# Performance work log

Measured on AMD Instinct MI355X. Metric: run time of the kernel, lower is better.

Reference implementation:

```python
import jax, jax.numpy as jnp
import numpy as np

H = 768   # encoder hidden size
NH = 4    # boundary attention heads
HD = H // NH
E = 9     # ent_type_size
R = 12    # rel_type_size
D = 64    # inner_dim
B = 4
S = 1024


def setup_inputs() -> dict:
    key = jax.random.key(0)
    ks = jax.random.split(key, 8)
    n = lambda k, shp: jax.random.normal(k, shp, jnp.float32) * 0.02
    return dict(
        hidden_states=jax.random.normal(ks[0], (B, S, H), jnp.float32),
        attention_mask=jnp.ones((B, S), jnp.float32),
        in_proj_w=n(ks[1], (3 * H, H)), in_proj_b=jnp.zeros((3 * H,), jnp.float32),
        out_proj_w=n(ks[2], (H, H)), out_proj_b=jnp.zeros((H,), jnp.float32),
        gate_w=n(ks[3], (H, H)), gate_b=jnp.zeros((H,), jnp.float32),
        ln_g=jnp.ones((H,), jnp.float32), ln_b=jnp.zeros((H,), jnp.float32),
        ent_w=n(ks[4], (E * 2 * D, H)), ent_b=jnp.zeros((E * 2 * D,), jnp.float32),
        prior_w=n(ks[5], (H, E)), prior_b=jnp.zeros((H,), jnp.float32),
        rel_w=n(ks[6], (R * 2 * D, 2 * H)), rel_b=jnp.zeros((R * 2 * D,), jnp.float32),
    )


def _sinusoidal_pos_emb(seq_len, dim, dtype):
    pos = jnp.arange(seq_len, dtype=dtype)[:, None]                 # [S,1]
    inv = jnp.power(jnp.asarray(10000.0, dtype), -2.0 * jnp.arange(dim // 2, dtype=dtype) / dim)
    ang = pos * inv                                                  # [S,D/2]
    emb = jnp.stack([jnp.sin(ang), jnp.cos(ang)], axis=-1).reshape(seq_len, dim)  # [sin0,cos0,sin1,cos1,...]
    return emb


def _gp_matrix(hs, W, b, mask):
    # hs: [B,S,Hin], W: [T*2D, Hin], mask: [B,S]
    bsz, seq_len, _ = hs.shape
    out = hs @ W.T + b                                               # [B,S,T*2D]
    T = out.shape[-1] // (2 * D)
    out = out.reshape(bsz, seq_len, T, 2 * D)
    qw, kw = out[..., :D], out[..., D:]                              # [B,S,T,D]
    # RoPE
    pe = _sinusoidal_pos_emb(seq_len, D, hs.dtype)                   # [S,D]
    cos = jnp.repeat(pe[:, 1::2], 2, axis=-1)[None, :, None, :]      # [1,S,1,D]
    sin = jnp.repeat(pe[:, ::2], 2, axis=-1)[None, :, None, :]

    def rot(x):
        x2 = jnp.stack([-x[..., 1::2], x[..., ::2]], axis=-1).reshape(x.shape)
        return x * cos + x2 * sin

    qw, kw = rot(qw), rot(kw)
    logits = jnp.einsum('bmtd,bntd->btmn', qw, kw)                   # [B,T,S,S]
    pad = mask[:, None, None, :]                                     # masks key dim
    logits = logits * pad - (1.0 - pad) * 1e12
    tril = jnp.tril(jnp.ones((seq_len, seq_len), logits.dtype), -1)
    logits = logits - tril * 1e12                                    # strictly lower triangle masked
    return logits / jnp.sqrt(jnp.asarray(D, logits.dtype))


def _boundary_attention(hs, mask, in_proj_w, in_proj_b, out_proj_w, out_proj_b,
                        gate_w, gate_b, ln_g, ln_b):
    bsz, seq_len, _ = hs.shape
    qkv = hs @ in_proj_w.T + in_proj_b                               # [B,S,3H]
    q, k, v = jnp.split(qkv, 3, axis=-1)
    q = q.reshape(bsz, seq_len, NH, HD)
    k = k.reshape(bsz, seq_len, NH, HD)
    v = v.reshape(bsz, seq_len, NH, HD)
    scores = jnp.einsum('bqhd,bkhd->bhqk', q, k) / jnp.sqrt(jnp.asarray(HD, hs.dtype))
    key_pad = (mask == 0)[:, None, None, :]                          # [B,1,1,S]
    scores = jnp.where(key_pad, jnp.asarray(-1e9, hs.dtype), scores)
    attn = jax.nn.softmax(scores, axis=-1)
    ctx = jnp.einsum('bhqk,bkhd->bqhd', attn, v).reshape(bsz, seq_len, H)
    attn_out = ctx @ out_proj_w.T + out_proj_b
    gate = jax.nn.sigmoid(attn_out @ gate_w.T + gate_b)
    x = hs + gate * attn_out
    mu = jnp.mean(x, axis=-1, keepdims=True)
    var = jnp.var(x, axis=-1, keepdims=True)
    return (x - mu) / jnp.sqrt(var + 1e-5) * ln_g + ln_b


def reference(hidden_states, attention_mask, in_proj_w, in_proj_b, out_proj_w, out_proj_b,
              gate_w, gate_b, ln_g, ln_b, ent_w, ent_b, prior_w, prior_b, rel_w, rel_b):
    enhanced = _boundary_attention(hidden_states, attention_mask, in_proj_w, in_proj_b,
                                   out_proj_w, out_proj_b, gate_w, gate_b, ln_g, ln_b)
    ent_logits = _gp_matrix(enhanced, ent_w, ent_b, attention_mask)  # [B,E,S,S]
    ent_prior = jnp.max(ent_logits, axis=-1)                          # [B,E,S]
    ent_prior = jnp.swapaxes(ent_prior, 1, 2)                         # [B,S,E]
    prior_feat = jax.nn.relu(ent_prior @ prior_w.T + prior_b)         # [B,S,H]
    rel_hidden = jnp.concatenate([enhanced, prior_feat], axis=-1)     # [B,S,2H]
    rel_logits = _gp_matrix(rel_hidden, rel_w, rel_b, attention_mask) # [B,R,S,S]
    return (ent_logits, rel_logits, enhanced)
```

## Files before the change

### kernel.cpp

```cpp
#include <hip/hip_runtime.h>
#include <math.h>

#define H_   768
#define NH_  4
#define HD_  192
#define E_   9
#define R_   12
#define D_   64
#define B_   4
#define S_   1024
#define H3_  (3 * H_)
#define MBS_ (B_ * S_)

typedef unsigned short u16;
typedef __attribute__((ext_vector_type(4))) int   i32x4;
typedef __attribute__((ext_vector_type(4))) float f32x4;

static const long OUT_REL_OFF = (long)B_ * E_ * S_ * S_;
static const long OUT_ENH_OFF = OUT_REL_OFF + (long)B_ * R_ * S_ * S_;

__device__ __forceinline__ u16 f2bf(float f) {
    unsigned u = __builtin_bit_cast(unsigned, f);
    return (u16)((u + 0x7fffu + ((u >> 16) & 1u)) >> 16);
}
__device__ __forceinline__ float bf2f(u16 h) {
    return __builtin_bit_cast(float, (unsigned)h << 16);
}
__device__ __forceinline__ void gload16(const u16* g, u16* l) {
    __builtin_amdgcn_global_load_lds(
        (__attribute__((address_space(1))) void*)g,
        (__attribute__((address_space(3))) void*)l, 16, 0, 0);
}
__device__ __forceinline__ void mfma_bf16(f32x4& acc, i32x4 a, i32x4 b) {
    asm volatile("v_mfma_f32_16x16x32_bf16 %0, %1, %2, %0"
                 : "+v"(acc) : "v"(a), "v"(b));
}

template<int BM, int BN, int EPI, int OBF, int PIPE>
__global__ __launch_bounds__(256) void gemm_mfma(
    const u16* __restrict__ A, const u16* __restrict__ Bw,
    const float* __restrict__ bias, void* __restrict__ Cv,
    int K, int lda, int ldb, int ldc, int nh,
    long sAb, long sAh, long sBb, long sBh, long sCb, long sCh,
    const float* __restrict__ mask, float scale, float* __restrict__ aux)
{
    constexpr int MI = BM / 32, NJ = BN / 32;
    constexpr int BUFE = (BM + BN) * 64;
    constexpr int LPS  = BM / 32 + BN / 32;
    const int z = blockIdx.z;
    const int zb = z / nh, zh = z - zb * nh;
    A  += zb * sAb + zh * sAh;
    Bw += zb * sBb + zh * sBh;

    const int gx = gridDim.x, gy = gridDim.y;
    int id = blockIdx.y * gx + blockIdx.x;
    const int nwg = gx * gy;
    if ((nwg & 7) == 0) id = (id & 7) * (nwg >> 3) + (id >> 3);
    const int bx = id % gx, by = id / gx;
    const int m0 = by * BM, n0 = bx * BN;

    __shared__ u16 lds[(PIPE ? 2 : 1) * BUFE];

    const int t = threadIdx.x;
    const int lane = t & 63, wid = t >> 6;
    const int wr = wid >> 1, wc = wid & 1;
    const int l16 = lane & 15, l4 = lane >> 4;

    auto stage = [&](int kt, u16* la) {
        u16* lb = la + BM * 64;
        const int k0 = kt << 6;
        #pragma unroll
        for (int i = 0; i < BM / 32; ++i) {
            const int e = i * 256 + t;
            const int row = e >> 3;
            const int c = ((e & 7) ^ (row & 7)) << 3;
            gload16(A + (long)(m0 + row) * lda + k0 + c, la + e * 8);
        }
        #pragma unroll
        for (int i = 0; i < BN / 32; ++i) {
            const int e = i * 256 + t;
            const int row = e >> 3;
            const int c = ((e & 7) ^ (row & 7)) << 3;
            gload16(Bw + (long)(n0 + row) * ldb + k0 + c, lb + e * 8);
        }
    };

    f32x4 acc[MI][NJ];
    #pragma unroll
    for (int mi = 0; mi < MI; ++mi)
        #pragma unroll
        for (int nj = 0; nj < NJ; ++nj)
            #pragma unroll
            for (int q = 0; q < 4; ++q) acc[mi][nj][q] = 0.0f;

    const int nt = K >> 6;

    if (PIPE == 0) {
        stage(0, lds);
        __syncthreads();
        const u16* la = lds;
        const u16* lb = lds + BM * 64;
        i32x4 af[MI][2], bfr[NJ][2];
        #pragma unroll
        for (int mi = 0; mi < MI; ++mi)
            #pragma unroll
            for (int kk = 0; kk < 2; ++kk) {
                const int row = wr * (BM / 2) + mi * 16 + l16;
                af[mi][kk] = *(const i32x4*)&la[row * 64 + ((((kk << 2) + l4) ^ (row & 7)) << 3)];
            }
        #pragma unroll
        for (int nj = 0; nj < NJ; ++nj)
            #pragma unroll
            for (int kk = 0; kk < 2; ++kk) {
                const int row = wc * (BN / 2) + nj * 16 + l16;
                bfr[nj][kk] = *(const i32x4*)&lb[row * 64 + ((((kk << 2) + l4) ^ (row & 7)) << 3)];
            }
        #pragma unroll
        for (int kk = 0; kk < 2; ++kk)
            #pragma unroll
            for (int mi = 0; mi < MI; ++mi)
                #pragma unroll
                for (int nj = 0; nj < NJ; ++nj)
                    mfma_bf16(acc[mi][nj], af[mi][kk], bfr[nj][kk]);
    } else {
        stage(0, lds);
        if (nt > 1) stage(1, lds + BUFE);
        for (int tt = 0; tt < nt; ++tt) {
            if (tt + 1 < nt) {
                if constexpr (LPS == 8) asm volatile("s_waitcnt vmcnt(8)" ::: "memory");
                else if constexpr (LPS == 7) asm volatile("s_waitcnt vmcnt(7)" ::: "memory");
                else if constexpr (LPS == 6) asm volatile("s_waitcnt vmcnt(6)" ::: "memory");
                else asm volatile("s_waitcnt vmcnt(5)" ::: "memory");
            } else {
                asm volatile("s_waitcnt vmcnt(0)" ::: "memory");
            }
            __builtin_amdgcn_s_barrier();
            u16* la = lds + (tt & 1) * BUFE;
            const u16* lb = la + BM * 64;
            i32x4 af[MI][2], bfr[NJ][2];
            #pragma unroll
            for (int mi = 0; mi < MI; ++mi)
                #pragma unroll
                for (int kk = 0; kk < 2; ++kk) {
                    const int row = wr * (BM / 2) + mi * 16 + l16;
                    af[mi][kk] = *(const i32x4*)&la[row * 64 + ((((kk << 2) + l4) ^ (row & 7)) << 3)];
                }
            #pragma unroll
            for (int nj = 0; nj < NJ; ++nj)
                #pragma unroll
                for (int kk = 0; kk < 2; ++kk) {
                    const int row = wc * (BN / 2) + nj * 16 + l16;
                    bfr[nj][kk] = *(const i32x4*)&lb[row * 64 + ((((kk << 2) + l4) ^ (row & 7)) << 3)];
                }
            asm volatile("s_waitcnt lgkmcnt(0)" ::: "memory");
            __builtin_amdgcn_sched_barrier(0);
            __builtin_amdgcn_s_barrier();
            if (tt + 2 < nt) stage(tt + 2, la);
            #pragma unroll
            for (int kk = 0; kk < 2; ++kk)
                #pragma unroll
                for (int mi = 0; mi < MI; ++mi)
                    #pragma unroll
                    for (int nj = 0; nj < NJ; ++nj)
                        mfma_bf16(acc[mi][nj], af[mi][kk], bfr[nj][kk]);
        }
        __syncthreads();
    }
    __builtin_amdgcn_sched_barrier(0);
    asm volatile("s_nop 7");
    asm volatile("s_nop 7");
    __builtin_amdgcn_sched_barrier(0);

    if (EPI == 1 || EPI == 3) mask += (long)zb * S_;
    const long cbase = zb * sCb + zh * sCh;

    float red[MI][4];
    if (EPI == 3) {
        #pragma unroll
        for (int mi = 0; mi < MI; ++mi)
            #pragma unroll
            for (int r = 0; r < 4; ++r) red[mi][r] = -INFINITY;
    }

    #pragma unroll
    for (int mi = 0; mi < MI; ++mi) {
        #pragma unroll
        for (int nj = 0; nj < NJ; ++nj) {
            const int gn = n0 + wc * (BN / 2) + nj * 16 + l16;
            const float bv = ((EPI == 0 || EPI == 4 || EPI == 7) && bias) ? bias[gn] : 0.0f;
            float invf = 0.0f;
            if (EPI == 4) invf = exp2f(-(float)((gn & 63) >> 1) * 0.41524101186092503f);
            #pragma unroll
            for (int r = 0; r < 4; ++r) {
                const int gm = m0 + wr * (BM / 2) + mi * 16 + l4 * 4 + r;
                float v = acc[mi][nj][r];
                const long cidx = cbase + (long)gm * ldc + gn;
                if (EPI == 0) {
                    v += bv;
                    if (OBF) ((u16*)Cv)[cidx] = f2bf(v);
                    else     ((float*)Cv)[cidx] = v;
                } else if (EPI == 7) {
                    v += bv;
                    const u16 bfv = f2bf(v);
                    ((u16*)Cv)[cidx] = bfv;
                    if (gn >= 2 * H_) {
                        const int hh = (gn - 2 * H_) / HD_;
                        const int dd = (gn - 2 * H_) - hh * HD_;
                        const int bb = gm >> 10, ss = gm & (S_ - 1);
                        ((u16*)aux)[((long)(bb * NH_ + hh) * HD_ + dd) * S_ + ss] = bfv;
                    }
                } else if (EPI == 1 || EPI == 3) {
                    const float pad = mask[gn];
                    v = v * pad - (1.0f - pad) * 1e12f;
                    if (gm > gn) v -= 1e12f;
                    v *= 0.125f;
                    ((float*)Cv)[cidx] = v;
                    if (EPI == 3) red[mi][r] = fmaxf(red[mi][r], v);
                } else {
                    v += bv;
                    const int sp = gm & (S_ - 1);
                    float sn, cs;
                    __sincosf((float)sp * invf, &sn, &cs);
                    const float pv = __shfl_xor(v, 1, 64);
                    v = (gn & 1) ? fmaf(v, cs, pv * sn) : fmaf(v, cs, -pv * sn);
                    ((u16*)Cv)[cidx] = f2bf(v);
                }
            }
        }
    }

    if (EPI == 3) {
        #pragma unroll
        for (int mi = 0; mi < MI; ++mi) {
            #pragma unroll
            for (int r = 0; r < 4; ++r) {
                float m = red[mi][r];
                m = fmaxf(m, __shfl_xor(m, 1, 64));
                m = fmaxf(m, __shfl_xor(m, 2, 64));
                m = fmaxf(m, __shfl_xor(m, 4, 64));
                m = fmaxf(m, __shfl_xor(m, 8, 64));
                if (l16 == 0) {
                    const int gm = m0 + wr * (BM / 2) + mi * 16 + l4 * 4 + r;
                    aux[((long)z * S_ + gm) * 16 + bx * 2 + wc] = m;
                }
            }
        }
    }
}

__global__ __launch_bounds__(256) void attn_fused(
    const u16* __restrict__ qkv, const u16* __restrict__ vt,
    const float* __restrict__ mask, u16* __restrict__ ctx, float qscale)
{
    const int z = blockIdx.y;
    const int b = z >> 2, h = z & 3;
    const int s0 = blockIdx.x * 64;
    const int t = threadIdx.x;
    const int lane = t & 63, wid = t >> 6;
    const int wr = wid >> 1, wc = wid & 1;
    const int l16 = lane & 15, l4 = lane >> 4;

    __shared__ u16 k_lds[64 * 192];
    __shared__ u16 v_lds[192 * 64];
    __shared__ u16 p_lds[64 * 64];
    __shared__ float rs_lds[2][64];

    i32x4 qf[2][6];
    {
        const u16* qb = qkv + (long)(b * S_ + s0 + wr * 32 + l16) * H3_ + h * HD_;
        #pragma unroll
        for (int mi = 0; mi < 2; ++mi)
            #pragma unroll
            for (int kk = 0; kk < 6; ++kk)
                qf[mi][kk] = *(const i32x4*)(qb + (long)mi * 16 * H3_ + kk * 32 + l4 * 8);
    }
    asm volatile("s_waitcnt vmcnt(0)" ::: "memory");

    f32x4 acc_c[2][6];
    #pragma unroll
    for (int mi = 0; mi < 2; ++mi)
        #pragma unroll
        for (int nj = 0; nj < 6; ++nj)
            #pragma unroll
            for (int q = 0; q < 4; ++q) acc_c[mi][nj][q] = 0.0f;
    float rs_acc[2][4] = {};

    const float* mrow = mask + (long)b * S_;

    for (int kt = 0; kt < 16; ++kt) {
        const int kv0 = kt * 64;
        #pragma unroll
        for (int i = 0; i < 6; ++i) {
            const int e = i * 256 + t;
            const int row = e / 24;
            const int g = e - row * 24;
            const int gs = (g & ~7) | ((g & 7) ^ (row & 7));
            gload16(qkv + (long)(b * S_ + kv0 + row) * H3_ + H_ + h * HD_ + gs * 8,
                    k_lds + e * 8);
        }
        #pragma unroll
        for (int i = 0; i < 6; ++i) {
            const int e = i * 256 + t;
            const int row = e >> 3, g = e & 7;
            const int gs = g ^ (row & 7);
            gload16(vt + ((long)z * HD_ + row) * S_ + kv0 + gs * 8,
                    v_lds + e * 8);
        }
        asm volatile("s_waitcnt vmcnt(6)" ::: "memory");
        __builtin_amdgcn_s_barrier();

        f32x4 acc_s[2][2];
        #pragma unroll
        for (int mi = 0; mi < 2; ++mi)
            #pragma unroll
            for (int nj = 0; nj < 2; ++nj)
                #pragma unroll
                for (int q = 0; q < 4; ++q) acc_s[mi][nj][q] = 0.0f;
        #pragma unroll
        for (int kk = 0; kk < 6; ++kk) {
            #pragma unroll
            for (int nj = 0; nj < 2; ++nj) {
                const int row = wc * 32 + nj * 16 + l16;
                const int g = kk * 4 + l4;
                const int gs = (g & ~7) | ((g & 7) ^ (row & 7));
                const i32x4 kf = *(const i32x4*)&k_lds[row * 192 + gs * 8];
                #pragma unroll
                for (int mi = 0; mi < 2; ++mi)
                    mfma_bf16(acc_s[mi][nj], qf[mi][kk], kf);
            }
        }
        __builtin_amdgcn_sched_barrier(0);
        asm volatile("s_nop 7");
        asm volatile("s_nop 7");
        __builtin_amdgcn_sched_barrier(0);

        float rsp[2][4] = {};
        #pragma unroll
        for (int mi = 0; mi < 2; ++mi) {
            #pragma unroll
            for (int nj = 0; nj < 2; ++nj) {
                const int coll = wc * 32 + nj * 16 + l16;
                const float mk = mrow[kv0 + coll];
                #pragma unroll
                for (int r = 0; r < 4; ++r) {
                    const int rowl = wr * 32 + mi * 16 + l4 * 4 + r;
                    float tv = 0.0f;
                    if (mk != 0.0f) tv = __expf(acc_s[mi][nj][r] * qscale);
                    const int gs = (coll >> 3) ^ (rowl & 7);
                    p_lds[rowl * 64 + gs * 8 + (coll & 7)] = f2bf(tv);
                    rsp[mi][r] += tv;
                }
            }
        }
        #pragma unroll
        for (int mi = 0; mi < 2; ++mi)
            #pragma unroll
            for (int r = 0; r < 4; ++r) {
                float v = rsp[mi][r];
                v += __shfl_xor(v, 1, 64);
                v += __shfl_xor(v, 2, 64);
                v += __shfl_xor(v, 4, 64);
                v += __shfl_xor(v, 8, 64);
                rs_acc[mi][r] += v;
            }

        asm volatile("s_waitcnt vmcnt(0)" ::: "memory");
        __builtin_amdgcn_s_barrier();

        #pragma unroll
        for (int kk = 0; kk < 2; ++kk) {
            i32x4 pf[2];
            #pragma unroll
            for (int mi = 0; mi < 2; ++mi) {
                const int row = wr * 32 + mi * 16 + l16;
                const int gs = (kk * 4 + l4) ^ (row & 7);
                pf[mi] = *(const i32x4*)&p_lds[row * 64 + gs * 8];
            }
            #pragma unroll
            for (int nj = 0; nj < 6; ++nj) {
                const int row = wc * 96 + nj * 16 + l16;
                const int gs = (kk * 4 + l4) ^ (row & 7);
                const i32x4 vf = *(const i32x4*)&v_lds[row * 64 + gs * 8];
                #pragma unroll
                for (int mi = 0; mi < 2; ++mi)
                    mfma_bf16(acc_c[mi][nj], pf[mi], vf);
            }
        }
        __builtin_amdgcn_s_barrier();
    }

    __builtin_amdgcn_sched_barrier(0);
    asm volatile("s_nop 7");
    asm volatile("s_nop 7");
    __builtin_amdgcn_sched_barrier(0);

    if (l16 == 0) {
        #pragma unroll
        for (int mi = 0; mi < 2; ++mi)
            #pragma unroll
            for (int r = 0; r < 4; ++r)
                rs_lds[wc][wr * 32 + mi * 16 + l4 * 4 + r] = rs_acc[mi][r];
    }
    __syncthreads();

    #pragma unroll
    for (int mi = 0; mi < 2; ++mi) {
        #pragma unroll
        for (int r = 0; r < 4; ++r) {
            const int rowl = wr * 32 + mi * 16 + l4 * 4 + r;
            const float inv = 1.0f / (rs_lds[0][rowl] + rs_lds[1][rowl]);
            #pragma unroll
            for (int nj = 0; nj < 6; ++nj) {
                const int d = wc * 96 + nj * 16 + l16;
                ctx[(long)(b * S_ + s0 + rowl) * H_ + h * HD_ + d] =
                    f2bf(acc_c[mi][nj][r] * inv);
            }
        }
    }
}

__global__ __launch_bounds__(256) void cast_all(
    const float* __restrict__ hs, const float* __restrict__ ipw,
    const float* __restrict__ opw, const float* __restrict__ gw,
    const float* __restrict__ entw, const float* __restrict__ relw,
    u16* hs_o, u16* ipw_o, u16* opw_o, u16* gw_o, u16* entw_o, u16* relw_o)
{
    const int blk = blockIdx.x;
    const float* in; u16* out; long base;
    if      (blk < 3072) { in = hs;   out = hs_o;   base = (long)blk * 1024; }
    else if (blk < 4800) { in = ipw;  out = ipw_o;  base = (long)(blk - 3072) * 1024; }
    else if (blk < 5376) { in = opw;  out = opw_o;  base = (long)(blk - 4800) * 1024; }
    else if (blk < 5952) { in = gw;   out = gw_o;   base = (long)(blk - 5376) * 1024; }
    else if (blk < 6816) { in = entw; out = entw_o; base = (long)(blk - 5952) * 1024; }
    else                 { in = relw; out = relw_o; base = (long)(blk - 6816) * 1024; }
    const long idx = base + (long)threadIdx.x * 4;
    const float4 v = *(const float4*)&in[idx];
    ushort4 o; o.x = f2bf(v.x); o.y = f2bf(v.y); o.z = f2bf(v.z); o.w = f2bf(v.w);
    *(ushort4*)&out[idx] = o;
}

__global__ __launch_bounds__(256) void gate_ln_bf(
    const float* __restrict__ hs, const u16* __restrict__ aogl,
    const float* __restrict__ g, const float* __restrict__ bta,
    float* __restrict__ enh, u16* __restrict__ relh)
{
    const long row = blockIdx.x;
    const float* hrow = hs + row * H_;
    const u16* arow = aogl + row * (2 * H_);
    const int tid = threadIdx.x;
    float x[3];
    float sum = 0.0f, sq = 0.0f;
    #pragma unroll
    for (int i = 0; i < 3; ++i) {
        const int j = tid + i * 256;
        const float a = bf2f(arow[j]);
        const float gt = 1.0f / (1.0f + __expf(-bf2f(arow[H_ + j])));
        const float xv = hrow[j] + gt * a;
        x[i] = xv; sum += xv; sq += xv * xv;
    }
    __shared__ float sm[8];
    #pragma unroll
    for (int o = 32; o > 0; o >>= 1) {
        sum += __shfl_xor(sum, o, 64);
        sq  += __shfl_xor(sq, o, 64);
    }
    const int lane = tid & 63, wid = tid >> 6;
    if (lane == 0) { sm[wid] = sum; sm[4 + wid] = sq; }
    __syncthreads();
    sum = sm[0] + sm[1] + sm[2] + sm[3];
    sq  = sm[4] + sm[5] + sm[6] + sm[7];
    const float mu = sum * (1.0f / (float)H_);
    float var = sq * (1.0f / (float)H_) - mu * mu;
    var = fmaxf(var, 0.0f);
    const float inv = 1.0f / sqrtf(var + 1e-5f);
    #pragma unroll
    for (int i = 0; i < 3; ++i) {
        const int j = tid + i * 256;
        const float o = (x[i] - mu) * inv * g[j] + bta[j];
        enh[row * H_ + j] = o;
        relh[row * (2 * H_) + j] = f2bf(o);
    }
}

__global__ __launch_bounds__(256) void prior_fused(
    const float* __restrict__ pmax, const float* __restrict__ pw,
    const float* __restrict__ pb, u16* __restrict__ relh)
{
    const int row = blockIdx.x;
    const int b = row >> 10, m = row & (S_ - 1);
    __shared__ float pr[E_];
    const int tid = threadIdx.x;
    if (tid < E_) {
        const float* pp = pmax + ((long)(b * E_ + tid) * S_ + m) * 16;
        float mx = -INFINITY;
        #pragma unroll
        for (int i = 0; i < 16; ++i) mx = fmaxf(mx, pp[i]);
        pr[tid] = mx;
    }
    __syncthreads();
    float p[E_];
    #pragma unroll
    for (int e = 0; e < E_; ++e) p[e] = pr[e];
    u16* orow = relh + (long)row * (2 * H_) + H_;
    #pragma unroll
    for (int i = 0; i < 3; ++i) {
        const int j = tid + i * 256;
        float a = pb[j];
        #pragma unroll
        for (int e = 0; e < E_; ++e) a = fmaf(p[e], pw[j * E_ + e], a);
        orow[j] = f2bf(fmaxf(a, 0.0f));
    }
}

extern "C" void kernel_launch(void* const* d_in, const int* in_sizes, int n_in,
                              void* d_out, int out_size, void* d_ws, size_t ws_size,
                              hipStream_t stream)
{
    const float* hs   = (const float*)d_in[0];
    const float* mask = (const float*)d_in[1];
    const float* ipw  = (const float*)d_in[2];
    const float* ipb  = (const float*)d_in[3];
    const float* opw  = (const float*)d_in[4];
    const float* opb  = (const float*)d_in[5];
    const float* gw   = (const float*)d_in[6];
    const float* gb   = (const float*)d_in[7];
    const float* lng  = (const float*)d_in[8];
    const float* lnb  = (const float*)d_in[9];
    const float* entw = (const float*)d_in[10];
    const float* entb = (const float*)d_in[11];
    const float* prw  = (const float*)d_in[12];
    const float* prb  = (const float*)d_in[13];
    const float* relw = (const float*)d_in[14];
    const float* relb = (const float*)d_in[15];
    float* out = (float*)d_out;
    char* base = (char*)d_ws;

    u16* ipw_bf  = (u16*)(base + 0);
    u16* opw_bf  = (u16*)(base + 3538944);
    u16* gw_bf   = (u16*)(base + 4718592);
    u16* entw_bf = (u16*)(base + 5898240);
    u16* relw_bf = (u16*)(base + 7667712);
    u16* hs_bf   = (u16*)(base + 12386304);
    u16* qkv_bf  = (u16*)(base + 18677760);
    u16* vt_bf   = (u16*)(base + 37552128);
    u16* ctx_bf  = (u16*)(base + 77398016);
    u16* aogl_bf = (u16*)(base + 83689472);
    float* bias2 = (float*)(base + 96272384);
    float* pmax  = (float*)(base + 97329152);
    u16* relh_bf = (u16*)(base + 43843584);
    u16* projr   = (u16*)(base + 56426496);
    float* enh   = out + OUT_ENH_OFF;

    const float qscale = 0.07216878364870323f;

    hipMemcpyAsync(bias2, opb, H_ * sizeof(float), hipMemcpyDeviceToDevice, stream);
    hipMemcpyAsync(bias2 + H_, gb, H_ * sizeof(float), hipMemcpyDeviceToDevice, stream);

    cast_all<<<9120, 256, 0, stream>>>(hs, ipw, opw, gw, entw, relw,
                                       hs_bf, ipw_bf, opw_bf, gw_bf, entw_bf, relw_bf);

    gemm_mfma<128,96,7,1,1><<<dim3(24, 32, 1), 256, 0, stream>>>(
        hs_bf, ipw_bf, ipb, qkv_bf, H_, H_, H_, H3_, 1,
        0,0,0,0,0,0, nullptr, 0.0f, (float*)vt_bf);

    attn_fused<<<dim3(16, 16), 256, 0, stream>>>(
        qkv_bf, vt_bf, mask, ctx_bf, qscale);

    gemm_mfma<128,96,0,1,1><<<dim3(16, 32, 1), 256, 0, stream>>>(
        ctx_bf, opw_bf, bias2, aogl_bf, H_, H_, H_, 2 * H_, 1,
        0,0,0,0,0,0, nullptr, 0.0f, nullptr);

    gate_ln_bf<<<MBS_, 256, 0, stream>>>(hs, aogl_bf, lng, lnb, enh, relh_bf);

    gemm_mfma<64,96,4,1,1><<<dim3(12, 64, 1), 256, 0, stream>>>(
        relh_bf, entw_bf, entb, projr, H_, 2 * H_, H_, E_ * 2 * D_, 1,
        0,0,0,0,0,0, nullptr, 0.0f, nullptr);

    gemm_mfma<128,128,3,0,0><<<dim3(8, 8, B_ * E_), 256, 0, stream>>>(
        projr, projr + D_, nullptr, out, D_, E_ * 2 * D_, E_ * 2 * D_, S_, E_,
        (long)S_ * E_ * 2 * D_, 2 * D_, (long)S_ * E_ * 2 * D_, 2 * D_,
        (long)E_ * S_ * S_, (long)S_ * S_, mask, 0.0f, pmax);

    prior_fused<<<MBS_, 256, 0, stream>>>(pmax, prw, prb, relh_bf);

    gemm_mfma<128,96,4,1,1><<<dim3(16, 32, 1), 256, 0, stream>>>(
        relh_bf, relw_bf, relb, projr, 2 * H_, 2 * H_, 2 * H_, R_ * 2 * D_, 1,
        0,0,0,0,0,0, nullptr, 0.0f, nullptr);

    gemm_mfma<128,128,1,0,0><<<dim3(8, 8, B_ * R_), 256, 0, stream>>>(
        projr, projr + D_, nullptr, out + OUT_REL_OFF, D_, R_ * 2 * D_, R_ * 2 * D_, S_, R_,
        (long)S_ * R_ * 2 * D_, 2 * D_, (long)S_ * R_ * 2 * D_, 2 * D_,
        (long)R_ * S_ * S_, (long)S_ * S_, mask, 0.0f, nullptr);

    (void)in_sizes; (void)n_in; (void)out_size; (void)ws_size;
}
```

Measured before the change: 257.6 us.

## Halve attention query tile to 32 rows and fold bias copies into cast kernel

The attention kernel now handles 32 query rows per block instead of 64, with each of the four waves owning a 16-column slice of the key tile and a 48-wide slice of the head dimension. This doubles the grid to 512 blocks to fill more compute units, at the cost of loading each K/V tile twice as often. The row-sum reduction is now done per element with shuffles, and the final normalisation combines four partial sums. The two device-to-device bias memcpys are replaced by two extra blocks in the cast kernel, removing separate copy operations from the stream.

Result: faster. 246.9 us (-4.1%).

```diff
diff --git a/kernel.cpp b/kernel.cpp
--- a/kernel.cpp
+++ b/kernel.cpp
@@ -254,20 +254,19 @@
 {
     const int z = blockIdx.y;
     const int b = z >> 2, h = z & 3;
-    const int s0 = blockIdx.x * 64;
+    const int s0 = blockIdx.x * 32;
     const int t = threadIdx.x;
-    const int lane = t & 63, wid = t >> 6;
-    const int wr = wid >> 1, wc = wid & 1;
+    const int lane = t & 63, w = t >> 6;
     const int l16 = lane & 15, l4 = lane >> 4;
 
     __shared__ u16 k_lds[64 * 192];
     __shared__ u16 v_lds[192 * 64];
-    __shared__ u16 p_lds[64 * 64];
-    __shared__ float rs_lds[2][64];
+    __shared__ u16 p_lds[32 * 64];
+    __shared__ float rs_lds[4][32];
 
     i32x4 qf[2][6];
     {
-        const u16* qb = qkv + (long)(b * S_ + s0 + wr * 32 + l16) * H3_ + h * HD_;
+        const u16* qb = qkv + (long)(b * S_ + s0 + l16) * H3_ + h * HD_;
         #pragma unroll
         for (int mi = 0; mi < 2; ++mi)
             #pragma unroll
@@ -276,11 +275,11 @@
     }
     asm volatile("s_waitcnt vmcnt(0)" ::: "memory");
 
-    f32x4 acc_c[2][6];
+    f32x4 acc_c[2][3];
     #pragma unroll
     for (int mi = 0; mi < 2; ++mi)
         #pragma unroll
-        for (int nj = 0; nj < 6; ++nj)
+        for (int nj = 0; nj < 3; ++nj)
             #pragma unroll
             for (int q = 0; q < 4; ++q) acc_c[mi][nj][q] = 0.0f;
     float rs_acc[2][4] = {};
@@ -309,62 +308,52 @@
         asm volatile("s_waitcnt vmcnt(6)" ::: "memory");
         __builtin_amdgcn_s_barrier();
 
-        f32x4 acc_s[2][2];
+        f32x4 acc_s[2];
         #pragma unroll
         for (int mi = 0; mi < 2; ++mi)
             #pragma unroll
-            for (int nj = 0; nj < 2; ++nj)
-                #pragma unroll
-                for (int q = 0; q < 4; ++q) acc_s[mi][nj][q] = 0.0f;
+            for (int q = 0; q < 4; ++q) acc_s[mi][q] = 0.0f;
         #pragma unroll
         for (int kk = 0; kk < 6; ++kk) {
-            #pragma unroll
-            for (int nj = 0; nj < 2; ++nj) {
-                const int row = wc * 32 + nj * 16 + l16;
-                const int g = kk * 4 + l4;
-                const int gs = (g & ~7) | ((g & 7) ^ (row & 7));
-                const i32x4 kf = *(const i32x4*)&k_lds[row * 192 + gs * 8];
-                #pragma unroll
-                for (int mi = 0; mi < 2; ++mi)
-                    mfma_bf16(acc_s[mi][nj], qf[mi][kk], kf);
-            }
+            const int krow = w * 16 + l16;
+            const int g = kk * 4 + l4;
+            const int gs = (g & ~7) | ((g & 7) ^ (krow & 7));
+            const i32x4 kf = *(const i32x4*)&k_lds[krow * 192 + gs * 8];
+            #pragma unroll
+            for (int mi = 0; mi < 2; ++mi)
+                mfma_bf16(acc_s[mi], qf[mi][kk], kf);
         }
         __builtin_amdgcn_sched_barrier(0);
         asm volatile("s_nop 7");
         asm volatile("s_nop 7");
         __builtin_amdgcn_sched_barrier(0);
 
-        float rsp[2][4] = {};
-        #pragma unroll
-        for (int mi = 0; mi < 2; ++mi) {
-            #pragma unroll
-            for (int nj = 0; nj < 2; ++nj) {
-                const int coll = wc * 32 + nj * 16 + l16;
-                const float mk = mrow[kv0 + coll];
+        {
+            const int coll = w * 16 + l16;
+            const float mk = mrow[kv0 + coll];
+            #pragma unroll
+            for (int mi = 0; mi < 2; ++mi) {
+                float rsp = 0.0f;
                 #pragma unroll
                 for (int r = 0; r < 4; ++r) {
-                    const int rowl = wr * 32 + mi * 16 + l4 * 4 + r;
+                    const int rowl = mi * 16 + l4 * 4 + r;
                     float tv = 0.0f;
-                    if (mk != 0.0f) tv = __expf(acc_s[mi][nj][r] * qscale);
+                    if (mk != 0.0f) tv = __expf(acc_s[mi][r] * qscale);
                     const int gs = (coll >> 3) ^ (rowl & 7);
                     p_lds[rowl * 64 + gs * 8 + (coll & 7)] = f2bf(tv);
-                    rsp[mi][r] += tv;
+                    rsp = tv;
+                    float v = rsp;
+                    v += __shfl_xor(v, 1, 64);
+                    v += __shfl_xor(v, 2, 64);
+                    v += __shfl_xor(v, 4, 64);
+                    v += __shfl_xor(v, 8, 64);
+                    rs_acc[mi][r] += v;
                 }
             }
         }
-        #pragma unroll
-        for (int mi = 0; mi < 2; ++mi)
-            #pragma unroll
-            for (int r = 0; r < 4; ++r) {
-                float v = rsp[mi][r];
-                v += __shfl_xor(v, 1, 64);
-                v += __shfl_xor(v, 2, 64);
-                v += __shfl_xor(v, 4, 64);
-                v += __shfl_xor(v, 8, 64);
-                rs_acc[mi][r] += v;
-            }
-
-        asm volatile("s_waitcnt vmcnt(0)" ::: "memory");
+
+        asm volatile("s_waitcnt vmcnt(0) lgkmcnt(0)" ::: "memory");
+        __builtin_amdgcn_sched_barrier(0);
         __builtin_amdgcn_s_barrier();
 
         #pragma unroll
@@ -372,13 +361,13 @@
             i32x4 pf[2];
             #pragma unroll
             for (int mi = 0; mi < 2; ++mi) {
-                const int row = wr * 32 + mi * 16 + l16;
+                const int row = mi * 16 + l16;
                 const int gs = (kk * 4 + l4) ^ (row & 7);
                 pf[mi] = *(const i32x4*)&p_lds[row * 64 + gs * 8];
             }
             #pragma unroll
-            for (int nj = 0; nj < 6; ++nj) {
-                const int row = wc * 96 + nj * 16 + l16;
+            for (int nj = 0; nj < 3; ++nj) {
+                const int row = w * 48 + nj * 16 + l16;
                 const int gs = (kk * 4 + l4) ^ (row & 7);
                 const i32x4 vf = *(const i32x4*)&v_lds[row * 64 + gs * 8];
                 #pragma unroll
@@ -399,7 +388,7 @@
         for (int mi = 0; mi < 2; ++mi)
             #pragma unroll
             for (int r = 0; r < 4; ++r)
-                rs_lds[wc][wr * 32 + mi * 16 + l4 * 4 + r] = rs_acc[mi][r];
+                rs_lds[w][mi * 16 + l4 * 4 + r] = rs_acc[mi][r];
     }
     __syncthreads();
 
@@ -407,11 +396,12 @@
     for (int mi = 0; mi < 2; ++mi) {
         #pragma unroll
         for (int r = 0; r < 4; ++r) {
-            const int rowl = wr * 32 + mi * 16 + l4 * 4 + r;
-            const float inv = 1.0f / (rs_lds[0][rowl] + rs_lds[1][rowl]);
-            #pragma unroll
-            for (int nj = 0; nj < 6; ++nj) {
-                const int d = wc * 96 + nj * 16 + l16;
+            const int rowl = mi * 16 + l4 * 4 + r;
+            const float inv = 1.0f / (rs_lds[0][rowl] + rs_lds[1][rowl] +
+                                      rs_lds[2][rowl] + rs_lds[3][rowl]);
+            #pragma unroll
+            for (int nj = 0; nj < 3; ++nj) {
+                const int d = w * 48 + nj * 16 + l16;
                 ctx[(long)(b * S_ + s0 + rowl) * H_ + h * HD_ + d] =
                     f2bf(acc_c[mi][nj][r] * inv);
             }
@@ -423,9 +413,18 @@
     const float* __restrict__ hs, const float* __restrict__ ipw,
     const float* __restrict__ opw, const float* __restrict__ gw,
     const float* __restrict__ entw, const float* __restrict__ relw,
-    u16* hs_o, u16* ipw_o, u16* opw_o, u16* gw_o, u16* entw_o, u16* relw_o)
+    const float* __restrict__ opb, const float* __restrict__ gb,
+    u16* hs_o, u16* ipw_o, u16* opw_o, u16* gw_o, u16* entw_o, u16* relw_o,
+    float* bias2)
 {
     const int blk = blockIdx.x;
+    if (blk >= 9120) {
+        const float* src = (blk == 9120) ? opb : gb;
+        float* dst = bias2 + (blk - 9120) * H_;
+        if (threadIdx.x < 192)
+            *(float4*)&dst[threadIdx.x * 4] = *(const float4*)&src[threadIdx.x * 4];
+        return;
+    }
     const float* in; u16* out; long base;
     if      (blk < 3072) { in = hs;   out = hs_o;   base = (long)blk * 1024; }
     else if (blk < 4800) { in = ipw;  out = ipw_o;  base = (long)(blk - 3072) * 1024; }
@@ -553,17 +552,15 @@
 
     const float qscale = 0.07216878364870323f;
 
-    hipMemcpyAsync(bias2, opb, H_ * sizeof(float), hipMemcpyDeviceToDevice, stream);
-    hipMemcpyAsync(bias2 + H_, gb, H_ * sizeof(float), hipMemcpyDeviceToDevice, stream);
-
-    cast_all<<<9120, 256, 0, stream>>>(hs, ipw, opw, gw, entw, relw,
-                                       hs_bf, ipw_bf, opw_bf, gw_bf, entw_bf, relw_bf);
+    cast_all<<<9122, 256, 0, stream>>>(hs, ipw, opw, gw, entw, relw, opb, gb,
+                                       hs_bf, ipw_bf, opw_bf, gw_bf, entw_bf, relw_bf,
+                                       bias2);
 
     gemm_mfma<128,96,7,1,1><<<dim3(24, 32, 1), 256, 0, stream>>>(
         hs_bf, ipw_bf, ipb, qkv_bf, H_, H_, H_, H3_, 1,
         0,0,0,0,0,0, nullptr, 0.0f, (float*)vt_bf);
 
-    attn_fused<<<dim3(16, 16), 256, 0, stream>>>(
+    attn_fused<<<dim3(32, 16), 256, 0, stream>>>(
         qkv_bf, vt_bf, mask, ctx_bf, qscale);
 
     gemm_mfma<128,96,0,1,1><<<dim3(16, 32, 1), 256, 0, stream>>>(
```
